# Optimization experiments

Measured on AMD Instinct MI355X. Metric: run time of the kernel, lower is better.

## Reference

```python
import jax, jax.numpy as jnp
import numpy as np

B, T, D = 4, 2048, 1024

def setup_inputs() -> dict:
    key = jax.random.key(0)
    kx, kq, kk, kv = jax.random.split(key, 4)
    return {
        "vector": jax.random.normal(kx, (B, T, D), dtype=jnp.float32),
        # original uses torch.rand -> uniform [0,1)
        "W_queries": jax.random.uniform(kq, (D, D), dtype=jnp.float32),
        "W_keys": jax.random.uniform(kk, (D, D), dtype=jnp.float32),
        "W_values": jax.random.uniform(kv, (D, D), dtype=jnp.float32),
    }

def reference(vector, W_queries, W_keys, W_values):
    b, num_token, d_out = vector.shape
    queries = vector @ W_queries          # [b, t, d]
    keys = vector @ W_keys                # [b, t, d]
    values = vector @ W_values            # [b, t, d]
    # attention_score: [b, q, k]
    scores = jnp.einsum('bqd,bkd->bqk', queries, keys)
    causal_mask = jnp.triu(jnp.ones((num_token, num_token), dtype=bool), k=1)
    scores = jnp.where(causal_mask[None, :, :], -jnp.inf, scores)
    # NOTE: original uses FLOOR division `//` by sqrt(d_k) -- faithful here.
    inv_sqrt_scale = jnp.asarray(np.sqrt(keys.shape[-1]), dtype=scores.dtype)
    weights = jnp.floor(scores / inv_sqrt_scale)
    # NOTE: original applies softmax over dim=1 (the query axis), not dim=-1.
    weights = jax.nn.softmax(weights, axis=1)
    # dropout rate is 0.0 (eval/deterministic): identity
    context = jnp.einsum('bqk,bkd->bqd', weights, values)
    return context
```

## Files before the change

kernel.cpp:

```cpp
#include <hip/hip_runtime.h>
#include <math.h>

typedef _Float16 half4 __attribute__((ext_vector_type(4)));
typedef _Float16 half8 __attribute__((ext_vector_type(8)));
typedef float f32x4 __attribute__((ext_vector_type(4)));

#define GLD16(gptr, lptr)                                                     \
    __builtin_amdgcn_global_load_lds(                                         \
        (const __attribute__((address_space(1))) unsigned int*)(gptr),        \
        (__attribute__((address_space(3))) unsigned int*)(lptr), 16, 0, 0)

#define PIPE_SYNC()                                                           \
    do {                                                                      \
        asm volatile("s_waitcnt vmcnt(0)" ::: "memory");                      \
        __builtin_amdgcn_s_barrier();                                         \
    } while (0)

namespace {

constexpr int Bb = 4;
constexpr int Tt = 2048;
constexpr int Dd = 1024;
constexpr int BT = Bb * Tt;
constexpr int NCH = 16;

__device__ inline _Float16 f2h(float f) { return (_Float16)f; }

__global__ __launch_bounds__(256) void convert_x_kernel(
    const float* __restrict__ X, _Float16* __restrict__ Xhi, _Float16* __restrict__ Xlo)
{
    const int idx = (blockIdx.x * 256 + threadIdx.x) * 4;
    const float4 v = *(const float4*)(X + idx);
    const float a[4] = {v.x, v.y, v.z, v.w};
    half4 h, l;
#pragma unroll
    for (int i = 0; i < 4; ++i) {
        h[i] = f2h(a[i]);
        l[i] = f2h(a[i] - (float)h[i]);
    }
    *(half4*)(Xhi + idx) = h;
    *(half4*)(Xlo + idx) = l;
}

__global__ __launch_bounds__(256) void convert_wqk_kernel(
    const float* __restrict__ Wq, const float* __restrict__ Wk,
    _Float16* __restrict__ Wqh, _Float16* __restrict__ Wql,
    _Float16* __restrict__ Wkh, _Float16* __restrict__ Wkl)
{
    const int mat = blockIdx.y;
    const float* W = mat ? Wk : Wq;
    _Float16* Hh = mat ? Wkh : Wqh;
    _Float16* Ll = mat ? Wkl : Wql;
    const int idx = (blockIdx.x * 256 + threadIdx.x) * 4;
    const float4 v = *(const float4*)(W + idx);
    const float a[4] = {v.x, v.y, v.z, v.w};
    half4 h, l;
#pragma unroll
    for (int i = 0; i < 4; ++i) {
        h[i] = f2h(a[i]);
        l[i] = f2h(a[i] - (float)h[i]);
    }
    *(half4*)(Hh + idx) = h;
    *(half4*)(Ll + idx) = l;
}

__global__ __launch_bounds__(256) void convert_wv_kernel(
    const float* __restrict__ Wv, _Float16* __restrict__ WvTh)
{
    __shared__ float tile[64][65];
    const int n0 = blockIdx.x * 64, k0 = blockIdx.y * 64;
    const int tx = threadIdx.x & 63, ty = threadIdx.x >> 6;
#pragma unroll
    for (int i = 0; i < 16; ++i)
        tile[ty + i * 4][tx] = Wv[(size_t)(k0 + ty + i * 4) * Dd + n0 + tx];
    __syncthreads();
#pragma unroll
    for (int i = 0; i < 16; ++i) {
        const float v = tile[tx][ty + i * 4];
        WvTh[(size_t)(n0 + ty + i * 4) * Dd + k0 + tx] = f2h(v);
    }
}

__global__ __launch_bounds__(256) void gt_kernel(
    const _Float16* __restrict__ Wkh, const _Float16* __restrict__ Wkl,
    const _Float16* __restrict__ Wqh, const _Float16* __restrict__ Wql,
    _Float16* __restrict__ GTh, _Float16* __restrict__ GTl)
{
    __shared__ _Float16 Ahl[2][2][4][512];
    __shared__ _Float16 Bhl[2][2][4][512];

    const int n0 = blockIdx.x * 64;
    const int m0 = blockIdx.y * 64;
    const int tid = threadIdx.x;
    const int w = tid >> 6, lane = tid & 63;
    const int lr = lane & 15, lq = lane >> 4;
    const int wi = (w >> 1) * 2, wj = (w & 1) * 2;

    f32x4 acc[2][2];
#pragma unroll
    for (int i = 0; i < 2; ++i)
#pragma unroll
        for (int j = 0; j < 2; ++j)
#pragma unroll
            for (int c = 0; c < 4; ++c) acc[i][j][c] = 0.f;

    auto stage = [&](int bf, int kk) {
        const int s = w;
        const size_t ar = (size_t)(m0 + s * 16 + lr) * Dd + kk + lq * 8;
        const size_t br = (size_t)(n0 + s * 16 + lr) * Dd + kk + lq * 8;
        GLD16(Wkh + ar, &Ahl[bf][0][s][0]);
        GLD16(Wkl + ar, &Ahl[bf][1][s][0]);
        GLD16(Wqh + br, &Bhl[bf][0][s][0]);
        GLD16(Wql + br, &Bhl[bf][1][s][0]);
    };

    stage(0, 0);
    PIPE_SYNC();
    int ib = 0;
    for (int kk = 0; kk < 1024; kk += 32, ib ^= 1) {
        if (kk + 32 < 1024) stage(ib ^ 1, kk + 32);
        half8 ah[2], al[2], bh[2], bl[2];
#pragma unroll
        for (int i = 0; i < 2; ++i) {
            ah[i] = *(const half8*)&Ahl[ib][0][wi + i][lane * 8];
            al[i] = *(const half8*)&Ahl[ib][1][wi + i][lane * 8];
        }
#pragma unroll
        for (int j = 0; j < 2; ++j) {
            bh[j] = *(const half8*)&Bhl[ib][0][wj + j][lane * 8];
            bl[j] = *(const half8*)&Bhl[ib][1][wj + j][lane * 8];
        }
#pragma unroll
        for (int i = 0; i < 2; ++i)
#pragma unroll
            for (int j = 0; j < 2; ++j) {
                acc[i][j] = __builtin_amdgcn_mfma_f32_16x16x32_f16(ah[i], bh[j], acc[i][j], 0, 0, 0);
                acc[i][j] = __builtin_amdgcn_mfma_f32_16x16x32_f16(ah[i], bl[j], acc[i][j], 0, 0, 0);
                acc[i][j] = __builtin_amdgcn_mfma_f32_16x16x32_f16(al[i], bh[j], acc[i][j], 0, 0, 0);
            }
        PIPE_SYNC();
    }

#pragma unroll
    for (int i = 0; i < 2; ++i)
#pragma unroll
        for (int r = 0; r < 4; ++r) {
            const int row = m0 + (wi + i) * 16 + lq * 4 + r;
#pragma unroll
            for (int j = 0; j < 2; ++j) {
                const int col = n0 + (wj + j) * 16 + lr;
                const float v = acc[i][j][r];
                const _Float16 h = f2h(v);
                GTh[(size_t)row * Dd + col] = h;
                GTl[(size_t)row * Dd + col] = f2h(v - (float)h);
            }
        }
}

__global__ __launch_bounds__(256) void t_kernel(
    const _Float16* __restrict__ Xhi, const _Float16* __restrict__ Xlo,
    const _Float16* __restrict__ GTh, const _Float16* __restrict__ GTl,
    _Float16* __restrict__ Thi, _Float16* __restrict__ Tlo)
{
    __shared__ _Float16 Ahl[2][2][8][512];
    __shared__ _Float16 Bhl[2][2][8][512];

    const int n0 = blockIdx.x * 128;
    const int m0 = blockIdx.y * 128;
    const int tid = threadIdx.x;
    const int w = tid >> 6, lane = tid & 63;
    const int lr = lane & 15, lq = lane >> 4;
    const int wr = (w >> 1) * 4, wc = (w & 1) * 4;

    f32x4 acc[4][4];
#pragma unroll
    for (int i = 0; i < 4; ++i)
#pragma unroll
        for (int j = 0; j < 4; ++j)
#pragma unroll
            for (int c = 0; c < 4; ++c) acc[i][j][c] = 0.f;

    auto stage = [&](int bf, int kk) {
#pragma unroll
        for (int s2 = 0; s2 < 2; ++s2) {
            const int s = w * 2 + s2;
            const size_t ar = (size_t)(m0 + s * 16 + lr) * Dd + kk + lq * 8;
            const size_t br = (size_t)(n0 + s * 16 + lr) * Dd + kk + lq * 8;
            GLD16(Xhi + ar, &Ahl[bf][0][s][0]);
            GLD16(Xlo + ar, &Ahl[bf][1][s][0]);
            GLD16(GTh + br, &Bhl[bf][0][s][0]);
            GLD16(GTl + br, &Bhl[bf][1][s][0]);
        }
    };

    stage(0, 0);
    PIPE_SYNC();
    int ib = 0;
    for (int kk = 0; kk < 1024; kk += 32, ib ^= 1) {
        if (kk + 32 < 1024) stage(ib ^ 1, kk + 32);
        half8 ah[4], al[4], bh[4], bl[4];
#pragma unroll
        for (int i = 0; i < 4; ++i) {
            ah[i] = *(const half8*)&Ahl[ib][0][wr + i][lane * 8];
            al[i] = *(const half8*)&Ahl[ib][1][wr + i][lane * 8];
        }
#pragma unroll
        for (int j = 0; j < 4; ++j) {
            bh[j] = *(const half8*)&Bhl[ib][0][wc + j][lane * 8];
            bl[j] = *(const half8*)&Bhl[ib][1][wc + j][lane * 8];
        }
#pragma unroll
        for (int i = 0; i < 4; ++i)
#pragma unroll
            for (int j = 0; j < 4; ++j) {
                acc[i][j] = __builtin_amdgcn_mfma_f32_16x16x32_f16(ah[i], bh[j], acc[i][j], 0, 0, 0);
                acc[i][j] = __builtin_amdgcn_mfma_f32_16x16x32_f16(ah[i], bl[j], acc[i][j], 0, 0, 0);
                acc[i][j] = __builtin_amdgcn_mfma_f32_16x16x32_f16(al[i], bh[j], acc[i][j], 0, 0, 0);
            }
        PIPE_SYNC();
    }
#pragma unroll
    for (int i = 0; i < 4; ++i)
#pragma unroll
        for (int r = 0; r < 4; ++r) {
            const int row = m0 + (wr + i) * 16 + lq * 4 + r;
#pragma unroll
            for (int j = 0; j < 4; ++j) {
                const int col = n0 + (wc + j) * 16 + lr;
                const float v = acc[i][j][r];
                const _Float16 h = f2h(v);
                Thi[(size_t)row * Dd + col] = h;
                Tlo[(size_t)row * Dd + col] = f2h(v - (float)h);
            }
        }
}

__global__ __launch_bounds__(256) void v_kernel(
    const _Float16* __restrict__ Xhi, const _Float16* __restrict__ WvTh,
    _Float16* __restrict__ Vrow)
{
    __shared__ _Float16 Al[2][8][512];
    __shared__ _Float16 Bl[2][8][512];

    const int n0 = blockIdx.x * 128;
    const int m0 = blockIdx.y * 128;
    const int tid = threadIdx.x;
    const int w = tid >> 6, lane = tid & 63;
    const int lr = lane & 15, lq = lane >> 4;
    const int wr = (w >> 1) * 4, wc = (w & 1) * 4;

    f32x4 acc[4][4];
#pragma unroll
    for (int i = 0; i < 4; ++i)
#pragma unroll
        for (int j = 0; j < 4; ++j)
#pragma unroll
            for (int c = 0; c < 4; ++c) acc[i][j][c] = 0.f;

    auto stage = [&](int bf, int kk) {
#pragma unroll
        for (int s2 = 0; s2 < 2; ++s2) {
            const int s = w * 2 + s2;
            GLD16(Xhi + (size_t)(m0 + s * 16 + lr) * Dd + kk + lq * 8, &Al[bf][s][0]);
            GLD16(WvTh + (size_t)(n0 + s * 16 + lr) * Dd + kk + lq * 8, &Bl[bf][s][0]);
        }
    };

    stage(0, 0);
    PIPE_SYNC();
    int ib = 0;
    for (int kk = 0; kk < 1024; kk += 32, ib ^= 1) {
        if (kk + 32 < 1024) stage(ib ^ 1, kk + 32);
        half8 a[4], b2[4];
#pragma unroll
        for (int i = 0; i < 4; ++i) a[i] = *(const half8*)&Al[ib][wr + i][lane * 8];
#pragma unroll
        for (int j = 0; j < 4; ++j) b2[j] = *(const half8*)&Bl[ib][wc + j][lane * 8];
#pragma unroll
        for (int i = 0; i < 4; ++i)
#pragma unroll
            for (int j = 0; j < 4; ++j)
                acc[i][j] = __builtin_amdgcn_mfma_f32_16x16x32_f16(a[i], b2[j], acc[i][j], 0, 0, 0);
        PIPE_SYNC();
    }
#pragma unroll
    for (int i = 0; i < 4; ++i)
#pragma unroll
        for (int r = 0; r < 4; ++r) {
            const int row = m0 + (wr + i) * 16 + lq * 4 + r;
#pragma unroll
            for (int j = 0; j < 4; ++j)
                Vrow[(size_t)row * Dd + n0 + (wc + j) * 16 + lr] = f2h(acc[i][j][r]);
        }
}

__global__ __launch_bounds__(256) void transpose_v_kernel(
    const _Float16* __restrict__ Vrow, const float* __restrict__ Lb,
    _Float16* __restrict__ Vt)
{
    __shared__ _Float16 tile[64][78];
    const int d0 = blockIdx.x * 64, t0 = blockIdx.y * 64, b = blockIdx.z;
    const int tx = threadIdx.x & 63, ty = threadIdx.x >> 6;
#pragma unroll
    for (int i = 0; i < 16; ++i)
        tile[ty + i * 4][tx] = Vrow[((size_t)b * Tt + t0 + ty + i * 4) * Dd + d0 + tx];
    __syncthreads();
    const float sc = Lb[(size_t)b * Tt + t0 + tx];
#pragma unroll
    for (int i = 0; i < 16; ++i) {
        const float v = (float)tile[tx][ty + i * 4] * sc;
        Vt[(size_t)b * Dd * Tt + (size_t)(d0 + ty + i * 4) * Tt + t0 + tx] = f2h(v);
    }
}

__global__ __launch_bounds__(256) void scores_mfma_kernel(
    const _Float16* __restrict__ Thi, const _Float16* __restrict__ Tlo,
    const _Float16* __restrict__ Xhi, const _Float16* __restrict__ Xlo,
    float* __restrict__ S, float* __restrict__ Pm, float* __restrict__ Pl)
{
    const int t = blockIdx.x;
    int byi = (int)((sqrtf(8.f * t + 1.f) - 1.f) * 0.5f);
    if ((byi + 1) * (byi + 2) / 2 <= t) ++byi;
    if (byi * (byi + 1) / 2 > t) --byi;
    const int bxi = t - byi * (byi + 1) / 2;
    const int b = blockIdx.z;
    const int j0 = bxi * 128, q0 = byi * 128;
    float* Sb = S + (size_t)b * Tt * Tt;

    __shared__ _Float16 Ahl[2][2][8][512];
    __shared__ _Float16 Bhl[2][2][8][512];
    const _Float16* Th = Thi + (size_t)b * Tt * Dd;
    const _Float16* Tl = Tlo + (size_t)b * Tt * Dd;
    const _Float16* Xh = Xhi + (size_t)b * Tt * Dd;
    const _Float16* Xl = Xlo + (size_t)b * Tt * Dd;

    const int tid = threadIdx.x;
    const int w = tid >> 6, lane = tid & 63;
    const int lr = lane & 15, lq = lane >> 4;
    const int wr = (w >> 1) * 4, wc = (w & 1) * 4;

    f32x4 acc[4][4];
#pragma unroll
    for (int i = 0; i < 4; ++i)
#pragma unroll
        for (int j = 0; j < 4; ++j)
#pragma unroll
            for (int c = 0; c < 4; ++c) acc[i][j][c] = 0.f;

    auto stage = [&](int bf, int kk) {
#pragma unroll
        for (int s2 = 0; s2 < 2; ++s2) {
            const int s = w * 2 + s2;
            const size_t ar = (size_t)(q0 + s * 16 + lr) * Dd + kk + lq * 8;
            const size_t br = (size_t)(j0 + s * 16 + lr) * Dd + kk + lq * 8;
            GLD16(Th + ar, &Ahl[bf][0][s][0]);
            GLD16(Tl + ar, &Ahl[bf][1][s][0]);
            GLD16(Xh + br, &Bhl[bf][0][s][0]);
            GLD16(Xl + br, &Bhl[bf][1][s][0]);
        }
    };

    stage(0, 0);
    PIPE_SYNC();
    int ib = 0;
    for (int kk = 0; kk < 1024; kk += 32, ib ^= 1) {
        if (kk + 32 < 1024) stage(ib ^ 1, kk + 32);
        half8 ah[4], al[4], bh[4], bl[4];
#pragma unroll
        for (int i = 0; i < 4; ++i) {
            ah[i] = *(const half8*)&Ahl[ib][0][wr + i][lane * 8];
            al[i] = *(const half8*)&Ahl[ib][1][wr + i][lane * 8];
        }
#pragma unroll
        for (int j = 0; j < 4; ++j) {
            bh[j] = *(const half8*)&Bhl[ib][0][wc + j][lane * 8];
            bl[j] = *(const half8*)&Bhl[ib][1][wc + j][lane * 8];
        }
#pragma unroll
        for (int i = 0; i < 4; ++i)
#pragma unroll
            for (int j = 0; j < 4; ++j) {
                acc[i][j] = __builtin_amdgcn_mfma_f32_16x16x32_f16(ah[i], bh[j], acc[i][j], 0, 0, 0);
                acc[i][j] = __builtin_amdgcn_mfma_f32_16x16x32_f16(ah[i], bl[j], acc[i][j], 0, 0, 0);
                acc[i][j] = __builtin_amdgcn_mfma_f32_16x16x32_f16(al[i], bh[j], acc[i][j], 0, 0, 0);
            }
        PIPE_SYNC();
    }

    float sv[4][4][4];
#pragma unroll
    for (int i = 0; i < 4; ++i)
#pragma unroll
        for (int r = 0; r < 4; ++r) {
            const int q = q0 + (wr + i) * 16 + lq * 4 + r;
#pragma unroll
            for (int j = 0; j < 4; ++j) {
                const int jg = j0 + (wc + j) * 16 + lr;
                const float v = (jg <= q) ? floorf(acc[i][j][r] * 0.03125f) : -INFINITY;
                sv[i][j][r] = v;
                Sb[(size_t)q * Tt + jg] = v;
            }
        }

    float* red  = (float*)&Ahl[0][0][0][0];
    float* colm = red + 2048;
    __syncthreads();
    for (int e = tid; e < 2048; e += 256) red[e] = -INFINITY;
    __syncthreads();
    const int rowidx = (w * 4 + lq) * 128;
#pragma unroll
    for (int j = 0; j < 4; ++j) {
        const int c = (wc + j) * 16 + lr;
        float lm = -INFINITY;
#pragma unroll
        for (int i = 0; i < 4; ++i)
#pragma unroll
            for (int r = 0; r < 4; ++r) lm = fmaxf(lm, sv[i][j][r]);
        red[rowidx + c] = lm;
    }
    __syncthreads();
    if (tid < 128) {
        float m = -INFINITY;
#pragma unroll
        for (int e = 0; e < 16; ++e) m = fmaxf(m, red[e * 128 + tid]);
        colm[tid] = m;
    }
    __syncthreads();
    float ls[4];
#pragma unroll
    for (int j = 0; j < 4; ++j) {
        const int c = (wc + j) * 16 + lr;
        const float m = colm[c];
        float s = 0.f;
#pragma unroll
        for (int i = 0; i < 4; ++i)
#pragma unroll
            for (int r = 0; r < 4; ++r)
                if (sv[i][j][r] != -INFINITY) s += __expf(sv[i][j][r] - m);
        ls[j] = s;
    }
    __syncthreads();
    for (int e = tid; e < 2048; e += 256) red[e] = 0.f;
    __syncthreads();
#pragma unroll
    for (int j = 0; j < 4; ++j) red[rowidx + (wc + j) * 16 + lr] = ls[j];
    __syncthreads();
    if (tid < 128) {
        float l = 0.f;
#pragma unroll
        for (int e = 0; e < 16; ++e) l += red[e * 128 + tid];
        const size_t o = ((size_t)b * NCH + byi) * Tt + j0 + tid;
        Pm[o] = colm[tid];
        Pl[o] = l;
    }
}

__global__ __launch_bounds__(256) void colstats_merge_kernel(
    const float* __restrict__ Pm, const float* __restrict__ Pl,
    float* __restrict__ Mb, float* __restrict__ Lb)
{
    const int j = blockIdx.x * 256 + threadIdx.x;
    const int b = blockIdx.y;
    const int jt = j >> 7;
    float m = -INFINITY, l = 0.f;
    for (int c = jt; c < NCH; ++c) {
        const size_t pidx = ((size_t)b * NCH + c) * Tt + j;
        const float mi = Pm[pidx];
        if (mi == -INFINITY) continue;
        const float li = Pl[pidx];
        if (mi > m) { l = l * __expf(m - mi) + li; m = mi; }
        else        { l += li * __expf(mi - m); }
    }
    Mb[(size_t)b * Tt + j] = m;
    Lb[(size_t)b * Tt + j] = (l > 0.f) ? 1.f / l : 0.f;
}

__global__ __launch_bounds__(256) void pmat_kernel(
    const float* __restrict__ S, const float* __restrict__ Mb,
    _Float16* __restrict__ P)
{
    const int t = blockIdx.x;
    int byi = (int)((sqrtf(8.f * t + 1.f) - 1.f) * 0.5f);
    if ((byi + 1) * (byi + 2) / 2 <= t) ++byi;
    if (byi * (byi + 1) / 2 > t) --byi;
    const int bxi = t - byi * (byi + 1) / 2;
    const int b = blockIdx.z;
    const int j0 = bxi * 128, q0 = byi * 128;

    const int tr = threadIdx.x >> 4;
    const int tc = (threadIdx.x & 15) * 8;
    const float* mp = Mb + (size_t)b * Tt + j0 + tc;
    float mv[8];
#pragma unroll
    for (int e = 0; e < 8; ++e) mv[e] = mp[e];

#pragma unroll
    for (int it = 0; it < 8; ++it) {
        const int row = q0 + it * 16 + tr;
        const float* Sp = S + (size_t)b * Tt * Tt + (size_t)row * Tt + j0 + tc;
        const float4 s0 = *(const float4*)Sp;
        const float4 s1 = *(const float4*)(Sp + 4);
        const float sa[8] = {s0.x, s0.y, s0.z, s0.w, s1.x, s1.y, s1.z, s1.w};
        half8 out;
#pragma unroll
        for (int e = 0; e < 8; ++e) {
            const int jg = j0 + tc + e;
            out[e] = (jg <= row) ? f2h(__expf(sa[e] - mv[e])) : (_Float16)0.f;
        }
        *(half8*)(P + (size_t)b * Tt * Tt + (size_t)row * Tt + j0 + tc) = out;
    }
}

__global__ __launch_bounds__(256) void context_mfma_kernel(
    const _Float16* __restrict__ P, const _Float16* __restrict__ Vt,
    float* __restrict__ Out)
{
    __shared__ _Float16 Al[2][8][512];
    __shared__ _Float16 Bl[2][8][512];

    const int bx = blockIdx.x;
    const int by = (int)gridDim.y - 1 - blockIdx.y;
    const int b  = blockIdx.z;
    const int d0 = bx * 128;
    const int q0 = by * 128;
    const _Float16* Pb = P + (size_t)b * Tt * Tt;
    const _Float16* Vb = Vt + (size_t)b * Dd * Tt;
    float* Ob = Out + (size_t)b * Tt * Dd;

    const int tid = threadIdx.x;
    const int w = tid >> 6, lane = tid & 63;
    const int lr = lane & 15, lq = lane >> 4;
    const int wr = (w >> 1) * 4, wc = (w & 1) * 4;

    f32x4 acc[4][4];
#pragma unroll
    for (int i = 0; i < 4; ++i)
#pragma unroll
        for (int j = 0; j < 4; ++j)
#pragma unroll
            for (int c = 0; c < 4; ++c) acc[i][j][c] = 0.f;

    auto stage = [&](int bf, int k0) {
#pragma unroll
        for (int s2 = 0; s2 < 2; ++s2) {
            const int s = w * 2 + s2;
            GLD16(Pb + (size_t)(q0 + s * 16 + lr) * Tt + k0 + lq * 8, &Al[bf][s][0]);
            GLD16(Vb + (size_t)(d0 + s * 16 + lr) * Tt + k0 + lq * 8, &Bl[bf][s][0]);
        }
    };

    const int kmax = q0 + 128;
    stage(0, 0);
    PIPE_SYNC();
    int ib = 0;
    for (int k0 = 0; k0 < kmax; k0 += 32, ib ^= 1) {
        if (k0 + 32 < kmax) stage(ib ^ 1, k0 + 32);
        half8 a[4], b2[4];
#pragma unroll
        for (int i = 0; i < 4; ++i) a[i] = *(const half8*)&Al[ib][wr + i][lane * 8];
#pragma unroll
        for (int j = 0; j < 4; ++j) b2[j] = *(const half8*)&Bl[ib][wc + j][lane * 8];
#pragma unroll
        for (int i = 0; i < 4; ++i)
#pragma unroll
            for (int j = 0; j < 4; ++j)
                acc[i][j] = __builtin_amdgcn_mfma_f32_16x16x32_f16(a[i], b2[j], acc[i][j], 0, 0, 0);
        PIPE_SYNC();
    }

#pragma unroll
    for (int i = 0; i < 4; ++i)
#pragma unroll
        for (int r = 0; r < 4; ++r) {
            const int row = q0 + (wr + i) * 16 + lq * 4 + r;
#pragma unroll
            for (int j = 0; j < 4; ++j)
                Ob[(size_t)row * Dd + d0 + (wc + j) * 16 + lr] = acc[i][j][r];
        }
}

}

extern "C" void kernel_launch(void* const* d_in, const int* in_sizes, int n_in,
                              void* d_out, int out_size, void* d_ws, size_t ws_size,
                              hipStream_t stream)
{
    const float* X  = (const float*)d_in[0];
    const float* Wq = (const float*)d_in[1];
    const float* Wk = (const float*)d_in[2];
    const float* Wv = (const float*)d_in[3];

    char* ws = (char*)d_ws;
    const size_t MB = 1024 * 1024;
    _Float16* Xhi  = (_Float16*)ws;
    _Float16* Xlo  = (_Float16*)(ws + 16 * MB);
    _Float16* Wqh  = (_Float16*)(ws + 32 * MB);
    _Float16* Wql  = (_Float16*)(ws + 34 * MB);
    _Float16* Wkh  = (_Float16*)(ws + 36 * MB);
    _Float16* Wkl  = (_Float16*)(ws + 38 * MB);
    _Float16* WvTh = (_Float16*)(ws + 40 * MB);
    _Float16* GTh  = (_Float16*)(ws + 44 * MB);
    _Float16* GTl  = (_Float16*)(ws + 46 * MB);
    _Float16* Thi  = (_Float16*)(ws + 48 * MB);
    _Float16* Tlo  = (_Float16*)(ws + 64 * MB);
    _Float16* P    = Thi;
    _Float16* Vt   = (_Float16*)(ws + 80 * MB);
    _Float16* Vrow = (_Float16*)(ws + 96 * MB);
    float*    S    = (float*)(ws + 112 * MB);
    float*    Mb   = (float*)(ws + 176 * MB);
    float*    Lb   = Mb + (size_t)Bb * Tt;
    float*    Pm   = Lb + (size_t)Bb * Tt;
    float*    Pl   = Pm + (size_t)Bb * NCH * Tt;
    float*    Out  = (float*)d_out;

    convert_x_kernel<<<BT * Dd / 1024, 256, 0, stream>>>(X, Xhi, Xlo);
    convert_wqk_kernel<<<dim3(Dd * Dd / 1024, 2), 256, 0, stream>>>(Wq, Wk, Wqh, Wql, Wkh, Wkl);
    convert_wv_kernel<<<dim3(16, 16), 256, 0, stream>>>(Wv, WvTh);
    gt_kernel<<<dim3(16, 16), 256, 0, stream>>>(Wkh, Wkl, Wqh, Wql, GTh, GTl);
    t_kernel<<<dim3(8, 64), 256, 0, stream>>>(Xhi, Xlo, GTh, GTl, Thi, Tlo);
    v_kernel<<<dim3(8, 64), 256, 0, stream>>>(Xhi, WvTh, Vrow);
    scores_mfma_kernel<<<dim3(136, 1, Bb), 256, 0, stream>>>(Thi, Tlo, Xhi, Xlo, S, Pm, Pl);
    colstats_merge_kernel<<<dim3(Tt / 256, Bb), 256, 0, stream>>>(Pm, Pl, Mb, Lb);
    transpose_v_kernel<<<dim3(Dd / 64, Tt / 64, Bb), 256, 0, stream>>>(Vrow, Lb, Vt);
    pmat_kernel<<<dim3(136, 1, Bb), 256, 0, stream>>>(S, Mb, P);
    context_mfma_kernel<<<dim3(Dd / 128, Tt / 128, Bb), 256, 0, stream>>>(P, Vt, Out);
}
```

Measured before the change: 451.6 us.

## Merge T and V projections into one launch and remap block order for XCD locality

After: 457.2 us. Within noise of the previous version (+1.2%).

```diff
diff --git a/kernel.cpp b/kernel.cpp
--- a/kernel.cpp
+++ b/kernel.cpp
@@ -157,16 +157,23 @@
         }
 }
 
-__global__ __launch_bounds__(256) void t_kernel(
+__global__ __launch_bounds__(256, 4) void tv_kernel(
     const _Float16* __restrict__ Xhi, const _Float16* __restrict__ Xlo,
     const _Float16* __restrict__ GTh, const _Float16* __restrict__ GTl,
-    _Float16* __restrict__ Thi, _Float16* __restrict__ Tlo)
-{
-    __shared__ _Float16 Ahl[2][2][8][512];
-    __shared__ _Float16 Bhl[2][2][8][512];
-
-    const int n0 = blockIdx.x * 128;
-    const int m0 = blockIdx.y * 128;
+    const _Float16* __restrict__ WvTh,
+    _Float16* __restrict__ Thi, _Float16* __restrict__ Tlo,
+    _Float16* __restrict__ Vrow)
+{
+    __shared__ _Float16 Ahl[2][8][512];
+    __shared__ _Float16 Bhl[2][8][512];
+
+    const int f  = blockIdx.x;
+    const int fp = (f & 7) * 128 + (f >> 3);
+    const int mb  = fp >> 4;
+    const int sub = fp & 15;
+    const int m0 = mb * 128;
+    const int n0 = (sub & 7) * 128;
+
     const int tid = threadIdx.x;
     const int w = tid >> 6, lane = tid & 63;
     const int lr = lane & 15, lq = lane >> 4;
@@ -180,118 +187,85 @@
 #pragma unroll
             for (int c = 0; c < 4; ++c) acc[i][j][c] = 0.f;
 
-    auto stage = [&](int bf, int kk) {
-#pragma unroll
-        for (int s2 = 0; s2 < 2; ++s2) {
-            const int s = w * 2 + s2;
-            const size_t ar = (size_t)(m0 + s * 16 + lr) * Dd + kk + lq * 8;
-            const size_t br = (size_t)(n0 + s * 16 + lr) * Dd + kk + lq * 8;
-            GLD16(Xhi + ar, &Ahl[bf][0][s][0]);
-            GLD16(Xlo + ar, &Ahl[bf][1][s][0]);
-            GLD16(GTh + br, &Bhl[bf][0][s][0]);
-            GLD16(GTl + br, &Bhl[bf][1][s][0]);
-        }
-    };
-
-    stage(0, 0);
-    PIPE_SYNC();
-    int ib = 0;
-    for (int kk = 0; kk < 1024; kk += 32, ib ^= 1) {
-        if (kk + 32 < 1024) stage(ib ^ 1, kk + 32);
-        half8 ah[4], al[4], bh[4], bl[4];
-#pragma unroll
-        for (int i = 0; i < 4; ++i) {
-            ah[i] = *(const half8*)&Ahl[ib][0][wr + i][lane * 8];
-            al[i] = *(const half8*)&Ahl[ib][1][wr + i][lane * 8];
-        }
-#pragma unroll
-        for (int j = 0; j < 4; ++j) {
-            bh[j] = *(const half8*)&Bhl[ib][0][wc + j][lane * 8];
-            bl[j] = *(const half8*)&Bhl[ib][1][wc + j][lane * 8];
+    if (sub < 8) {
+        for (int kk = 0; kk < 1024; kk += 32) {
+            __syncthreads();
+#pragma unroll
+            for (int s2 = 0; s2 < 2; ++s2) {
+                const int s = w * 2 + s2;
+                const size_t ar = (size_t)(m0 + s * 16 + lr) * Dd + kk + lq * 8;
+                const size_t br = (size_t)(n0 + s * 16 + lr) * Dd + kk + lq * 8;
+                GLD16(Xhi + ar, &Ahl[0][s][0]);
+                GLD16(Xlo + ar, &Ahl[1][s][0]);
+                GLD16(GTh + br, &Bhl[0][s][0]);
+                GLD16(GTl + br, &Bhl[1][s][0]);
+            }
+            __syncthreads();
+            half8 ah[4], al[4], bh[4], bl[4];
+#pragma unroll
+            for (int i = 0; i < 4; ++i) {
+                ah[i] = *(const half8*)&Ahl[0][wr + i][lane * 8];
+                al[i] = *(const half8*)&Ahl[1][wr + i][lane * 8];
+            }
+#pragma unroll
+            for (int j = 0; j < 4; ++j) {
+                bh[j] = *(const half8*)&Bhl[0][wc + j][lane * 8];
+                bl[j] = *(const half8*)&Bhl[1][wc + j][lane * 8];
+            }
+#pragma unroll
+            for (int i = 0; i < 4; ++i)
+#pragma unroll
+                for (int j = 0; j < 4; ++j) {
+                    acc[i][j] = __builtin_amdgcn_mfma_f32_16x16x32_f16(ah[i], bh[j], acc[i][j], 0, 0, 0);
+                    acc[i][j] = __builtin_amdgcn_mfma_f32_16x16x32_f16(ah[i], bl[j], acc[i][j], 0, 0, 0);
+                    acc[i][j] = __builtin_amdgcn_mfma_f32_16x16x32_f16(al[i], bh[j], acc[i][j], 0, 0, 0);
+                }
         }
 #pragma unroll
         for (int i = 0; i < 4; ++i)
 #pragma unroll
-            for (int j = 0; j < 4; ++j) {
-                acc[i][j] = __builtin_amdgcn_mfma_f32_16x16x32_f16(ah[i], bh[j], acc[i][j], 0, 0, 0);
-                acc[i][j] = __builtin_amdgcn_mfma_f32_16x16x32_f16(ah[i], bl[j], acc[i][j], 0, 0, 0);
-                acc[i][j] = __builtin_amdgcn_mfma_f32_16x16x32_f16(al[i], bh[j], acc[i][j], 0, 0, 0);
-            }
-        PIPE_SYNC();
-    }
-#pragma unroll
-    for (int i = 0; i < 4; ++i)
-#pragma unroll
-        for (int r = 0; r < 4; ++r) {
-            const int row = m0 + (wr + i) * 16 + lq * 4 + r;
-#pragma unroll
-            for (int j = 0; j < 4; ++j) {
-                const int col = n0 + (wc + j) * 16 + lr;
-                const float v = acc[i][j][r];
-                const _Float16 h = f2h(v);
-                Thi[(size_t)row * Dd + col] = h;
-                Tlo[(size_t)row * Dd + col] = f2h(v - (float)h);
-            }
-        }
-}
-
-__global__ __launch_bounds__(256) void v_kernel(
-    const _Float16* __restrict__ Xhi, const _Float16* __restrict__ WvTh,
-    _Float16* __restrict__ Vrow)
-{
-    __shared__ _Float16 Al[2][8][512];
-    __shared__ _Float16 Bl[2][8][512];
-
-    const int n0 = blockIdx.x * 128;
-    const int m0 = blockIdx.y * 128;
-    const int tid = threadIdx.x;
-    const int w = tid >> 6, lane = tid & 63;
-    const int lr = lane & 15, lq = lane >> 4;
-    const int wr = (w >> 1) * 4, wc = (w & 1) * 4;
-
-    f32x4 acc[4][4];
-#pragma unroll
-    for (int i = 0; i < 4; ++i)
-#pragma unroll
-        for (int j = 0; j < 4; ++j)
-#pragma unroll
-            for (int c = 0; c < 4; ++c) acc[i][j][c] = 0.f;
-
-    auto stage = [&](int bf, int kk) {
-#pragma unroll
-        for (int s2 = 0; s2 < 2; ++s2) {
-            const int s = w * 2 + s2;
-            GLD16(Xhi + (size_t)(m0 + s * 16 + lr) * Dd + kk + lq * 8, &Al[bf][s][0]);
-            GLD16(WvTh + (size_t)(n0 + s * 16 + lr) * Dd + kk + lq * 8, &Bl[bf][s][0]);
-        }
-    };
-
-    stage(0, 0);
-    PIPE_SYNC();
-    int ib = 0;
-    for (int kk = 0; kk < 1024; kk += 32, ib ^= 1) {
-        if (kk + 32 < 1024) stage(ib ^ 1, kk + 32);
-        half8 a[4], b2[4];
-#pragma unroll
-        for (int i = 0; i < 4; ++i) a[i] = *(const half8*)&Al[ib][wr + i][lane * 8];
-#pragma unroll
-        for (int j = 0; j < 4; ++j) b2[j] = *(const half8*)&Bl[ib][wc + j][lane * 8];
+            for (int r = 0; r < 4; ++r) {
+                const int row = m0 + (wr + i) * 16 + lq * 4 + r;
+#pragma unroll
+                for (int j = 0; j < 4; ++j) {
+                    const int col = n0 + (wc + j) * 16 + lr;
+                    const float v = acc[i][j][r];
+                    const _Float16 h = f2h(v);
+                    Thi[(size_t)row * Dd + col] = h;
+                    Tlo[(size_t)row * Dd + col] = f2h(v - (float)h);
+                }
+            }
+    } else {
+        for (int kk = 0; kk < 1024; kk += 32) {
+            __syncthreads();
+#pragma unroll
+            for (int s2 = 0; s2 < 2; ++s2) {
+                const int s = w * 2 + s2;
+                GLD16(Xhi + (size_t)(m0 + s * 16 + lr) * Dd + kk + lq * 8, &Ahl[0][s][0]);
+                GLD16(WvTh + (size_t)(n0 + s * 16 + lr) * Dd + kk + lq * 8, &Bhl[0][s][0]);
+            }
+            __syncthreads();
+            half8 a[4], b2[4];
+#pragma unroll
+            for (int i = 0; i < 4; ++i) a[i] = *(const half8*)&Ahl[0][wr + i][lane * 8];
+#pragma unroll
+            for (int j = 0; j < 4; ++j) b2[j] = *(const half8*)&Bhl[0][wc + j][lane * 8];
+#pragma unroll
+            for (int i = 0; i < 4; ++i)
+#pragma unroll
+                for (int j = 0; j < 4; ++j)
+                    acc[i][j] = __builtin_amdgcn_mfma_f32_16x16x32_f16(a[i], b2[j], acc[i][j], 0, 0, 0);
+        }
 #pragma unroll
         for (int i = 0; i < 4; ++i)
 #pragma unroll
-            for (int j = 0; j < 4; ++j)
-                acc[i][j] = __builtin_amdgcn_mfma_f32_16x16x32_f16(a[i], b2[j], acc[i][j], 0, 0, 0);
-        PIPE_SYNC();
-    }
-#pragma unroll
-    for (int i = 0; i < 4; ++i)
-#pragma unroll
-        for (int r = 0; r < 4; ++r) {
-            const int row = m0 + (wr + i) * 16 + lq * 4 + r;
-#pragma unroll
-            for (int j = 0; j < 4; ++j)
-                Vrow[(size_t)row * Dd + n0 + (wc + j) * 16 + lr] = f2h(acc[i][j][r]);
-        }
+            for (int r = 0; r < 4; ++r) {
+                const int row = m0 + (wr + i) * 16 + lq * 4 + r;
+#pragma unroll
+                for (int j = 0; j < 4; ++j)
+                    Vrow[(size_t)row * Dd + n0 + (wc + j) * 16 + lr] = f2h(acc[i][j][r]);
+            }
+    }
 }
 
 __global__ __launch_bounds__(256) void transpose_v_kernel(
@@ -318,12 +292,14 @@
     const _Float16* __restrict__ Xhi, const _Float16* __restrict__ Xlo,
     float* __restrict__ S, float* __restrict__ Pm, float* __restrict__ Pl)
 {
-    const int t = blockIdx.x;
+    const int f  = blockIdx.x;
+    const int fp = (f & 7) * 68 + (f >> 3);
+    const int b = fp / 136;
+    const int t = fp - b * 136;
     int byi = (int)((sqrtf(8.f * t + 1.f) - 1.f) * 0.5f);
     if ((byi + 1) * (byi + 2) / 2 <= t) ++byi;
     if (byi * (byi + 1) / 2 > t) --byi;
     const int bxi = t - byi * (byi + 1) / 2;
-    const int b = blockIdx.z;
     const int j0 = bxi * 128, q0 = byi * 128;
     float* Sb = S + (size_t)b * Tt * Tt;
 
@@ -518,9 +494,13 @@
     __shared__ _Float16 Al[2][8][512];
     __shared__ _Float16 Bl[2][8][512];
 
-    const int bx = blockIdx.x;
-    const int by = (int)gridDim.y - 1 - blockIdx.y;
-    const int b  = blockIdx.z;
+    const int f  = blockIdx.x;
+    const int fp = (f & 7) * 64 + (f >> 3);
+    const int b  = fp >> 7;
+    const int r  = fp & 127;
+    const int bx = r & 7;
+    const int tq = r >> 3;
+    const int by = (tq & 1) ? (15 - (tq >> 1)) : (tq >> 1);
     const int d0 = bx * 128;
     const int q0 = by * 128;
     const _Float16* Pb = P + (size_t)b * Tt * Tt;
@@ -571,11 +551,11 @@
 #pragma unroll
     for (int i = 0; i < 4; ++i)
 #pragma unroll
-        for (int r = 0; r < 4; ++r) {
-            const int row = q0 + (wr + i) * 16 + lq * 4 + r;
+        for (int r2 = 0; r2 < 4; ++r2) {
+            const int row = q0 + (wr + i) * 16 + lq * 4 + r2;
 #pragma unroll
             for (int j = 0; j < 4; ++j)
-                Ob[(size_t)row * Dd + d0 + (wc + j) * 16 + lr] = acc[i][j][r];
+                Ob[(size_t)row * Dd + d0 + (wc + j) * 16 + lr] = acc[i][j][r2];
         }
 }
 
@@ -617,11 +597,10 @@
     convert_wqk_kernel<<<dim3(Dd * Dd / 1024, 2), 256, 0, stream>>>(Wq, Wk, Wqh, Wql, Wkh, Wkl);
     convert_wv_kernel<<<dim3(16, 16), 256, 0, stream>>>(Wv, WvTh);
     gt_kernel<<<dim3(16, 16), 256, 0, stream>>>(Wkh, Wkl, Wqh, Wql, GTh, GTl);
-    t_kernel<<<dim3(8, 64), 256, 0, stream>>>(Xhi, Xlo, GTh, GTl, Thi, Tlo);
-    v_kernel<<<dim3(8, 64), 256, 0, stream>>>(Xhi, WvTh, Vrow);
-    scores_mfma_kernel<<<dim3(136, 1, Bb), 256, 0, stream>>>(Thi, Tlo, Xhi, Xlo, S, Pm, Pl);
+    tv_kernel<<<dim3(1024), 256, 0, stream>>>(Xhi, Xlo, GTh, GTl, WvTh, Thi, Tlo, Vrow);
+    scores_mfma_kernel<<<dim3(544), 256, 0, stream>>>(Thi, Tlo, Xhi, Xlo, S, Pm, Pl);
     colstats_merge_kernel<<<dim3(Tt / 256, Bb), 256, 0, stream>>>(Pm, Pl, Mb, Lb);
     transpose_v_kernel<<<dim3(Dd / 64, Tt / 64, Bb), 256, 0, stream>>>(Vrow, Lb, Vt);
     pmat_kernel<<<dim3(136, 1, Bb), 256, 0, stream>>>(S, Mb, P);
-    context_mfma_kernel<<<dim3(Dd / 128, Tt / 128, Bb), 256, 0, stream>>>(P, Vt, Out);
-}
+    context_mfma_kernel<<<dim3(512), 256, 0, stream>>>(P, Vt, Out);
+}
```
